# Optimization experiments

Measured on AMD Instinct MI355X. Metric: run time of the kernel, lower is better.

The kernel has to match this reference:

```python
import jax, jax.numpy as jnp
import numpy as np

B, S, D = 2, 4096, 1024

def setup_inputs() -> dict:
    key = jax.random.key(0)
    k1, k2 = jax.random.split(key)
    x = jax.random.normal(k1, (B, S, D), dtype=jnp.float32)
    W = jax.random.normal(k2, (D, 3 * D), dtype=jnp.float32) * (1.0 / np.sqrt(D))
    b = jnp.zeros((3 * D,), dtype=jnp.float32)
    return {"x": x, "W": W, "b": b}

def reference(x, W, b) -> jnp.ndarray:
    D_ = x.shape[-1]
    qkv = x @ W + b                       # [B, S, 3D]
    q, k, v = jnp.split(qkv, 3, axis=2)    # each [B, S, D]
    scale = 1.0 / jnp.sqrt(jnp.asarray(D_, dtype=x.dtype))
    scores = jnp.einsum('bqd,bkd->bqk', q, k) * scale  # [B, S, S]
    weights = jax.nn.softmax(scores, axis=-1)
    return jnp.einsum('bqk,bkd->bqd', weights, v)       # [B, S, D]
```

## Files before the change

### kernel.cpp

```cpp
#include <hip/hip_runtime.h>
#include <hip/hip_bf16.h>

typedef __attribute__((ext_vector_type(4))) float  f32x4;
typedef __attribute__((ext_vector_type(8))) __bf16 bf16x8;
typedef __attribute__((ext_vector_type(8))) unsigned short u16x8;

typedef const __attribute__((address_space(1))) void gas_void;
typedef __attribute__((address_space(3))) void las_void;

__device__ __forceinline__ unsigned short f2bf(float x) {
    unsigned u = __builtin_bit_cast(unsigned, x);
    u += 0x7fffu + ((u >> 16) & 1u);
    return (unsigned short)(u >> 16);
}
__device__ __forceinline__ float bf2f(unsigned short h) {
    unsigned u = ((unsigned)h) << 16;
    return __builtin_bit_cast(float, u);
}
__device__ __forceinline__ void gload_lds16(const void* g, void* l) {
    __builtin_amdgcn_global_load_lds((gas_void*)g, (las_void*)l, 16, 0, 0);
}

#define WAITVM(N) asm volatile("s_waitcnt vmcnt(" #N ")" ::: "memory")
#define BAR() do { __builtin_amdgcn_s_barrier(); __builtin_amdgcn_sched_barrier(0); } while (0)

__global__ void k_f32_to_bf16(const float* __restrict__ in,
                              unsigned short* __restrict__ out, int n4) {
    int i = blockIdx.x * blockDim.x + threadIdx.x;
    if (i < n4) {
        float4 v = ((const float4*)in)[i];
        ushort4 o;
        o.x = f2bf(v.x); o.y = f2bf(v.y); o.z = f2bf(v.z); o.w = f2bf(v.w);
        ((ushort4*)out)[i] = o;
    }
}

__global__ void k_transpose_w(const float* __restrict__ W,
                              unsigned short* __restrict__ Wt,
                              int K, int N) {
    __shared__ unsigned short tile[32][33];
    int n0 = blockIdx.x * 32, k0 = blockIdx.y * 32;
    int tx = threadIdx.x, ty = threadIdx.y;
#pragma unroll
    for (int i = 0; i < 4; i++) {
        int kk = ty + i * 8;
        tile[kk][tx] = f2bf(W[(size_t)(k0 + kk) * N + n0 + tx]);
    }
    __syncthreads();
#pragma unroll
    for (int i = 0; i < 4; i++) {
        int nn = ty + i * 8;
        Wt[(size_t)(n0 + nn) * K + k0 + tx] = tile[tx][nn];
    }
}

__global__ __launch_bounds__(256, 2) void k_g128qkv(
        const unsigned short* __restrict__ A, int lda,
        const unsigned short* __restrict__ Bt, int ldb,
        unsigned short* __restrict__ C,
        unsigned short* __restrict__ Vt,
        const float* __restrict__ bias, int K) {
    __shared__ __align__(16) unsigned short As[2][8192];
    __shared__ __align__(16) unsigned short Bs[2][8192];

    const int nwg  = gridDim.x * gridDim.y;
    const int flat = blockIdx.y * gridDim.x + blockIdx.x;
    const int swzb = (flat & 7) * (nwg >> 3) + (flat >> 3);
    const int m0   = (swzb / gridDim.x) * 128;
    const int n0   = (swzb % gridDim.x) * 128;

    const int tid  = threadIdx.x;
    const int lane = tid & 63;
    const int wid  = tid >> 6;
    const int wr   = wid >> 1;
    const int wc   = wid & 1;
    const int l15  = lane & 15;
    const int l4   = lane >> 4;

    f32x4 acc[4][4] = {};

    const int srow = tid >> 3;
    const int kel  = (((lane & 7) ^ (lane >> 3)) << 3);
    const int c0 = (l4 << 4) ^ ((l15 & 7) << 4);
    const int c1 = (64 + (l4 << 4)) ^ ((l15 & 7) << 4);

    auto stA = [&](int b, int g, int kt) {
        gload_lds16(A + (size_t)(m0 + g * 32 + srow) * lda + kt * 64 + kel,
                    (char*)As + b * 16384 + g * 4096 + (wid << 10));
    };
    auto stB = [&](int b, int g, int kt) {
        gload_lds16(Bt + (size_t)(n0 + g * 32 + srow) * ldb + kt * 64 + kel,
                    (char*)Bs + b * 16384 + g * 4096 + (wid << 10));
    };

#define MM(I, J, X, Y) \
    acc[I][J] = __builtin_amdgcn_mfma_f32_16x16x32_bf16((X), (Y), acc[I][J], 0, 0, 0)

    const int NT = K >> 6;
    stA(0, 0, 0); stA(0, 1, 0); stA(0, 2, 0); stA(0, 3, 0);
    stB(0, 0, 0); stB(0, 1, 0); stB(0, 2, 0); stB(0, 3, 0);

    for (int t = 0; t < NT; t++) {
        const int cur = t & 1, nxt = cur ^ 1;
        const char* Ab = (const char*)As + cur * 16384;
        const char* Bb = (const char*)Bs + cur * 16384;
        const bool hn = (t + 1 < NT);

        bf16x8 af[4], bq[4];

        if (hn) {
            stA(nxt, 0, t + 1); stA(nxt, 1, t + 1); stA(nxt, 2, t + 1); stA(nxt, 3, t + 1);
            WAITVM(4);
        } else {
            WAITVM(0);
        }
        BAR();
#pragma unroll
        for (int mf = 0; mf < 4; mf++)
            af[mf] = *(const bf16x8*)(Ab + (wr * 64 + mf * 16 + l15) * 128 + c0);
#pragma unroll
        for (int nf = 0; nf < 4; nf++)
            bq[nf] = *(const bf16x8*)(Bb + (wc * 64 + nf * 16 + l15) * 128 + c0);
        __builtin_amdgcn_s_setprio(1);
#pragma unroll
        for (int mf = 0; mf < 4; mf++)
#pragma unroll
        for (int nf = 0; nf < 4; nf++)
            MM(mf, nf, af[mf], bq[nf]);
        __builtin_amdgcn_s_setprio(0);

        if (hn) {
            stB(nxt, 0, t + 1); stB(nxt, 1, t + 1); stB(nxt, 2, t + 1); stB(nxt, 3, t + 1);
        }
#pragma unroll
        for (int mf = 0; mf < 4; mf++)
            af[mf] = *(const bf16x8*)(Ab + (wr * 64 + mf * 16 + l15) * 128 + c1);
#pragma unroll
        for (int nf = 0; nf < 4; nf++)
            bq[nf] = *(const bf16x8*)(Bb + (wc * 64 + nf * 16 + l15) * 128 + c1);
        __builtin_amdgcn_s_setprio(1);
#pragma unroll
        for (int mf = 0; mf < 4; mf++)
#pragma unroll
        for (int nf = 0; nf < 4; nf++)
            MM(mf, nf, af[mf], bq[nf]);
        __builtin_amdgcn_s_setprio(0);
        BAR();
    }
#undef MM

#pragma unroll
    for (int mf = 0; mf < 4; mf++) {
        const int row = m0 + wr * 64 + mf * 16 + l4 * 4;
#pragma unroll
        for (int nf = 0; nf < 4; nf++) {
            const int col = n0 + wc * 64 + nf * 16 + l15;
            const f32x4 av = acc[mf][nf];
            const float bv = bias[col];
            const int lc = col & 1023;
            if (col < 2048) {
#pragma unroll
                for (int r = 0; r < 4; r++)
                    C[(size_t)(col >> 10) * 8388608 +
                      (size_t)(row + r) * 1024 + lc] = f2bf(av[r] + bv);
            } else {
                const int b = row >> 12, s = row & 4095;
                ushort4 o;
                o.x = f2bf(av[0] + bv); o.y = f2bf(av[1] + bv);
                o.z = f2bf(av[2] + bv); o.w = f2bf(av[3] + bv);
                *(ushort4*)&Vt[(size_t)b * 4194304 + (size_t)lc * 4096 + s] = o;
            }
        }
    }
}

__global__ __launch_bounds__(512, 2) void k_scores(
        const unsigned short* __restrict__ A,
        const unsigned short* __restrict__ Bt,
        unsigned short* __restrict__ C,
        float* __restrict__ part,
        int K, float scale, long sA, long sB, long sC) {
    __shared__ __align__(16) unsigned short As[2][16384];
    __shared__ __align__(16) unsigned short Bs[2][16384];

    const int z = blockIdx.z;
    A  += (size_t)z * sA;
    Bt += (size_t)z * sB;

    const int nwg  = gridDim.x * gridDim.y;
    const int flat = blockIdx.y * gridDim.x + blockIdx.x;
    const int swzb = (flat & 7) * (nwg >> 3) + (flat >> 3);
    const int m0   = (swzb / gridDim.x) * 256;
    const int n0   = (swzb % gridDim.x) * 256;

    const int tid  = threadIdx.x;
    const int lane = tid & 63;
    const int wid  = tid >> 6;
    const int wm   = wid >> 2;
    const int wn   = wid & 3;
    const int l15  = lane & 15;
    const int l4   = lane >> 4;

    f32x4 acc[8][4] = {};

    const int srow = tid >> 3;
    const int kel  = (((lane & 7) ^ (lane >> 3)) << 3);
    const int c0 = ((l4 << 4)) ^ ((l15 & 7) << 4);
    const int c1 = (64 + (l4 << 4)) ^ ((l15 & 7) << 4);

    auto stageA = [&](int b, int h, int kt) {
#pragma unroll
        for (int c = 0; c < 2; c++) {
            const int r = h * 128 + c * 64 + srow;
            gload_lds16(A + (size_t)(m0 + r) * 1024 + kt * 64 + kel,
                        (char*)As + b * 32768 + h * 16384 + c * 8192 + (wid << 10));
        }
    };
    auto stageB = [&](int b, int h, int kt) {
#pragma unroll
        for (int c = 0; c < 2; c++) {
            const int r = h * 128 + c * 64 + srow;
            gload_lds16(Bt + (size_t)(n0 + r) * 1024 + kt * 64 + kel,
                        (char*)Bs + b * 32768 + h * 16384 + c * 8192 + (wid << 10));
        }
    };

#define MM(I, J, X, Y) \
    acc[I][J] = __builtin_amdgcn_mfma_f32_16x16x32_bf16((X), (Y), acc[I][J], 0, 0, 0)

    const int NT = K >> 6;
    stageA(0, 0, 0); stageB(0, 0, 0); stageA(0, 1, 0); stageB(0, 1, 0);

    for (int t = 0; t < NT; t++) {
        const int cur = t & 1, nxt = cur ^ 1;
        const char* Ab = (const char*)As + cur * 32768;
        const char* Bb = (const char*)Bs + cur * 32768;

        if (t + 1 < NT) {
            stageA(nxt, 0, t + 1); stageB(nxt, 0, t + 1);
            WAITVM(4);
        } else {
            WAITVM(0);
        }
        BAR();

        bf16x8 bfrg[2][2][2];
#pragma unroll
        for (int qn = 0; qn < 2; qn++)
#pragma unroll
        for (int nf = 0; nf < 2; nf++) {
            const int rb = (wn * 64 + qn * 32 + nf * 16 + l15) * 128;
            bfrg[qn][nf][0] = *(const bf16x8*)(Bb + rb + c0);
            bfrg[qn][nf][1] = *(const bf16x8*)(Bb + rb + c1);
        }
        {
            bf16x8 af[4][2];
#pragma unroll
            for (int mf = 0; mf < 4; mf++) {
                const int ra = (wm * 128 + 0 * 64 + mf * 16 + l15) * 128;
                af[mf][0] = *(const bf16x8*)(Ab + ra + c0);
                af[mf][1] = *(const bf16x8*)(Ab + ra + c1);
            }
            __builtin_amdgcn_s_setprio(1);
#pragma unroll
            for (int mf = 0; mf < 4; mf++)
#pragma unroll
            for (int qn = 0; qn < 2; qn++)
#pragma unroll
            for (int nf = 0; nf < 2; nf++) {
                MM(mf, qn * 2 + nf, af[mf][0], bfrg[qn][nf][0]);
                MM(mf, qn * 2 + nf, af[mf][1], bfrg[qn][nf][1]);
            }
            __builtin_amdgcn_s_setprio(0);
        }

        if (t + 1 < NT) { stageA(nxt, 1, t + 1); stageB(nxt, 1, t + 1); }
        {
            bf16x8 af[4][2];
#pragma unroll
            for (int mf = 0; mf < 4; mf++) {
                const int ra = (wm * 128 + 1 * 64 + mf * 16 + l15) * 128;
                af[mf][0] = *(const bf16x8*)(Ab + ra + c0);
                af[mf][1] = *(const bf16x8*)(Ab + ra + c1);
            }
            __builtin_amdgcn_s_setprio(1);
#pragma unroll
            for (int mf = 0; mf < 4; mf++)
#pragma unroll
            for (int qn = 0; qn < 2; qn++)
#pragma unroll
            for (int nf = 0; nf < 2; nf++) {
                MM(4 + mf, qn * 2 + nf, af[mf][0], bfrg[qn][nf][0]);
                MM(4 + mf, qn * 2 + nf, af[mf][1], bfrg[qn][nf][1]);
            }
            __builtin_amdgcn_s_setprio(0);
        }
        __builtin_amdgcn_s_barrier();
        __builtin_amdgcn_sched_barrier(0);
    }
#undef MM

    const int cb4 = ((n0 >> 8) << 2) + wn;
#pragma unroll
    for (int qm = 0; qm < 2; qm++)
#pragma unroll
    for (int mf = 0; mf < 4; mf++) {
        const int row = m0 + wm * 128 + qm * 64 + mf * 16 + l4 * 4;
        float rs[4] = {0.f, 0.f, 0.f, 0.f};
#pragma unroll
        for (int qn = 0; qn < 2; qn++)
#pragma unroll
        for (int nf = 0; nf < 2; nf++) {
            const int col = n0 + wn * 64 + qn * 32 + nf * 16 + l15;
            const f32x4 av = acc[qm * 4 + mf][qn * 2 + nf];
#pragma unroll
            for (int r = 0; r < 4; r++) {
                const float e = __expf(av[r] * scale);
                rs[r] += e;
                C[(size_t)z * sC + (size_t)(row + r) * 4096 + col] = f2bf(e);
            }
        }
#pragma unroll
        for (int r = 0; r < 4; r++) {
#pragma unroll
            for (int o = 1; o < 16; o <<= 1)
                rs[r] += __shfl_xor(rs[r], o);
        }
        if (l15 == 0) {
#pragma unroll
            for (int r = 0; r < 4; r++)
                part[((size_t)z * 4096 + row + r) * 64 + cb4] = rs[r];
        }
    }
}

__global__ __launch_bounds__(256) void k_rinv(const float* __restrict__ part,
                                              float* __restrict__ rinv, int nrows) {
    int row = blockIdx.x * blockDim.x + threadIdx.x;
    if (row < nrows) {
        const float* p = part + (size_t)row * 64;
        float s = 0.f;
#pragma unroll
        for (int i = 0; i < 16; i++) {
            f32x4 v = *(const f32x4*)(p + i * 4);
            s += v[0] + v[1] + v[2] + v[3];
        }
        rinv[row] = 1.0f / s;
    }
}

__global__ __launch_bounds__(512, 2) void k_pv256(
        const unsigned short* __restrict__ A,
        const unsigned short* __restrict__ Bt,
        float* __restrict__ C,
        const float* __restrict__ rinv,
        int K, long sA, long sB, long sC) {
    __shared__ __align__(16) unsigned short As[2][16384];
    __shared__ __align__(16) unsigned short Bs[2][8192];

    const int z = blockIdx.z;
    A  += (size_t)z * sA;
    Bt += (size_t)z * sB;

    const int nwg  = gridDim.x * gridDim.y;
    const int flat = blockIdx.y * gridDim.x + blockIdx.x;
    const int swzb = (flat & 7) * (nwg >> 3) + (flat >> 3);
    const int m0   = (swzb / gridDim.x) * 256;
    const int n0   = (swzb % gridDim.x) * 128;

    const int tid  = threadIdx.x;
    const int lane = tid & 63;
    const int wid  = tid >> 6;
    const int wm   = wid >> 2;
    const int wn   = wid & 3;
    const int l15  = lane & 15;
    const int l4   = lane >> 4;

    f32x4 acc[8][2] = {};

    const int srow = tid >> 3;
    const int kel  = (((lane & 7) ^ (lane >> 3)) << 3);
    const int c0 = ((l4 << 4)) ^ ((l15 & 7) << 4);
    const int c1 = (64 + (l4 << 4)) ^ ((l15 & 7) << 4);

    auto stageA1 = [&](int b, int a, int kt) {
        const int r = a * 64 + srow;
        gload_lds16(A + (size_t)(m0 + r) * 4096 + kt * 64 + kel,
                    (char*)As + b * 32768 + a * 8192 + (wid << 10));
    };
    auto stageB1 = [&](int b, int c, int kt) {
        const int r = c * 64 + srow;
        gload_lds16(Bt + (size_t)(n0 + r) * 4096 + kt * 64 + kel,
                    (char*)Bs + b * 16384 + c * 8192 + (wid << 10));
    };

#define MM(I, J, X, Y) \
    acc[I][J] = __builtin_amdgcn_mfma_f32_16x16x32_bf16((X), (Y), acc[I][J], 0, 0, 0)

    const int NT = K >> 6;
    stageA1(0, 0, 0); stageA1(0, 1, 0); stageA1(0, 2, 0); stageA1(0, 3, 0);
    stageB1(0, 0, 0); stageB1(0, 1, 0);

    for (int t = 0; t < NT; t++) {
        const int cur = t & 1, nxt = cur ^ 1;
        const char* Ab = (const char*)As + cur * 32768;
        const char* Bb = (const char*)Bs + cur * 16384;

        if (t + 1 < NT) {
            stageA1(nxt, 0, t + 1); stageA1(nxt, 1, t + 1); stageB1(nxt, 0, t + 1);
            WAITVM(3);
        } else {
            WAITVM(0);
        }
        BAR();

        bf16x8 bfrg[2][2];
#pragma unroll
        for (int nf = 0; nf < 2; nf++) {
            const int rb = (wn * 32 + nf * 16 + l15) * 128;
            bfrg[nf][0] = *(const bf16x8*)(Bb + rb + c0);
            bfrg[nf][1] = *(const bf16x8*)(Bb + rb + c1);
        }
        {
            bf16x8 af[4][2];
#pragma unroll
            for (int mf = 0; mf < 4; mf++) {
                const int ra = (wm * 128 + 0 * 64 + mf * 16 + l15) * 128;
                af[mf][0] = *(const bf16x8*)(Ab + ra + c0);
                af[mf][1] = *(const bf16x8*)(Ab + ra + c1);
            }
            __builtin_amdgcn_s_setprio(1);
#pragma unroll
            for (int mf = 0; mf < 4; mf++)
#pragma unroll
            for (int nf = 0; nf < 2; nf++) {
                MM(mf, nf, af[mf][0], bfrg[nf][0]);
                MM(mf, nf, af[mf][1], bfrg[nf][1]);
            }
            __builtin_amdgcn_s_setprio(0);
        }

        if (t + 1 < NT) {
            stageA1(nxt, 2, t + 1); stageA1(nxt, 3, t + 1); stageB1(nxt, 1, t + 1);
        }
        {
            bf16x8 af[4][2];
#pragma unroll
            for (int mf = 0; mf < 4; mf++) {
                const int ra = (wm * 128 + 1 * 64 + mf * 16 + l15) * 128;
                af[mf][0] = *(const bf16x8*)(Ab + ra + c0);
                af[mf][1] = *(const bf16x8*)(Ab + ra + c1);
            }
            __builtin_amdgcn_s_setprio(1);
#pragma unroll
            for (int mf = 0; mf < 4; mf++)
#pragma unroll
            for (int nf = 0; nf < 2; nf++) {
                MM(4 + mf, nf, af[mf][0], bfrg[nf][0]);
                MM(4 + mf, nf, af[mf][1], bfrg[nf][1]);
            }
            __builtin_amdgcn_s_setprio(0);
        }
        __builtin_amdgcn_s_barrier();
        __builtin_amdgcn_sched_barrier(0);
    }
#undef MM

#pragma unroll
    for (int qm = 0; qm < 2; qm++)
#pragma unroll
    for (int mf = 0; mf < 4; mf++) {
        const int row = m0 + wm * 128 + qm * 64 + mf * 16 + l4 * 4;
        const f32x4 riv = *(const f32x4*)&rinv[(size_t)z * 4096 + row];
#pragma unroll
        for (int nf = 0; nf < 2; nf++) {
            const int col = n0 + wn * 32 + nf * 16 + l15;
            const f32x4 av = acc[qm * 4 + mf][nf];
#pragma unroll
            for (int r = 0; r < 4; r++)
                C[(size_t)z * sC + (size_t)(row + r) * 1024 + col] = av[r] * riv[r];
        }
    }
}

extern "C" void kernel_launch(void* const* d_in, const int* in_sizes, int n_in,
                              void* d_out, int out_size, void* d_ws, size_t ws_size,
                              hipStream_t stream) {
    const float* x    = (const float*)d_in[0];
    const float* W    = (const float*)d_in[1];
    const float* bias = (const float*)d_in[2];
    float* out        = (float*)d_out;

    char* ws = (char*)d_ws;
    unsigned short* Qb   = (unsigned short*)(ws);
    unsigned short* Vt   = (unsigned short*)(ws + 33554432);
    unsigned short* xb   = (unsigned short*)(ws + 50331648);
    unsigned short* Wt   = (unsigned short*)(ws + 67108864);
    unsigned short* Pcat = (unsigned short*)(ws + 50331648);
    float*          part = (float*)(ws + 117440512);
    float*          rinv = (float*)(ws + 121634816);

    k_f32_to_bf16<<<8192, 256, 0, stream>>>(x, xb, (8192 * 1024) / 4);
    k_transpose_w<<<dim3(96, 32), dim3(32, 8), 0, stream>>>(W, Wt, 1024, 3072);
    k_g128qkv<<<dim3(24, 64), 256, 0, stream>>>(xb, 1024, Wt, 1024, Qb, Vt, bias, 1024);

    const float scale = 0.03125f;
    k_scores<<<dim3(16, 16, 2), 512, 0, stream>>>(
        Qb, Qb + 8388608, Pcat, part, 1024, scale, 4194304, 4194304, 16777216);
    k_rinv<<<32, 256, 0, stream>>>(part, rinv, 8192);
    k_pv256<<<dim3(8, 16, 2), 512, 0, stream>>>(
        Pcat, Vt, out, rinv, 4096, 16777216, 4194304, 4194304);
}
```

Baseline: 266.1 us.

## Restructure scores GEMM main loop into eight-phase interleaved load/compute schedule

Replaces the two-half double-buffered k-loop of the QK^T scores kernel with an 8-phase schedule over two k-tiles per iteration. Each phase computes one quadrant of the output tile while a slice of the next tiles is staged into LDS. The LDS staging layout is remapped so each half-buffer holds the rows a quadrant needs. This aims to spread global-to-LDS loads evenly across MFMA work and hide memory latency better. The cost is more barriers per k-step, and correctness depends on the new buffer and waitcnt bookkeeping.

Measured after the change: 272.1 us. 1.02x slower.

```diff
diff --git a/kernel.cpp b/kernel.cpp
--- a/kernel.cpp
+++ b/kernel.cpp
@@ -174,7 +174,7 @@
     }
 }
 
-__global__ __launch_bounds__(512, 2) void k_scores(
+__global__ __launch_bounds__(512, 2) void k_scores8(
         const unsigned short* __restrict__ A,
         const unsigned short* __restrict__ Bt,
         unsigned short* __restrict__ C,
@@ -203,102 +203,86 @@
 
     f32x4 acc[8][4] = {};
 
-    const int srow = tid >> 3;
-    const int kel  = (((lane & 7) ^ (lane >> 3)) << 3);
-    const int c0 = ((l4 << 4)) ^ ((l15 & 7) << 4);
+    const int kel = (((lane & 7) ^ (lane >> 3)) << 3);
+    const int c0 = (l4 << 4) ^ ((l15 & 7) << 4);
     const int c1 = (64 + (l4 << 4)) ^ ((l15 & 7) << 4);
 
-    auto stageA = [&](int b, int h, int kt) {
+    auto stA = [&](int b, int h, int kt) {
 #pragma unroll
         for (int c = 0; c < 2; c++) {
-            const int r = h * 128 + c * 64 + srow;
-            gload_lds16(A + (size_t)(m0 + r) * 1024 + kt * 64 + kel,
+            const int r = c * 64 + (tid >> 3);
+            const int grow = m0 + ((r >> 6) << 7) + h * 64 + (r & 63);
+            gload_lds16(A + (size_t)grow * 1024 + kt * 64 + kel,
                         (char*)As + b * 32768 + h * 16384 + c * 8192 + (wid << 10));
         }
     };
-    auto stageB = [&](int b, int h, int kt) {
+    auto stB = [&](int b, int h, int kt) {
 #pragma unroll
         for (int c = 0; c < 2; c++) {
-            const int r = h * 128 + c * 64 + srow;
-            gload_lds16(Bt + (size_t)(n0 + r) * 1024 + kt * 64 + kel,
+            const int r = c * 64 + (tid >> 3);
+            const int gcol = n0 + (((r >> 5) & 3) << 6) + h * 32 + (r & 31);
+            gload_lds16(Bt + (size_t)gcol * 1024 + kt * 64 + kel,
                         (char*)Bs + b * 32768 + h * 16384 + c * 8192 + (wid << 10));
         }
     };
 
-#define MM(I, J, X, Y) \
+#define MMp(I, J, X, Y) \
     acc[I][J] = __builtin_amdgcn_mfma_f32_16x16x32_bf16((X), (Y), acc[I][J], 0, 0, 0)
 
-    const int NT = K >> 6;
-    stageA(0, 0, 0); stageB(0, 0, 0); stageA(0, 1, 0); stageB(0, 1, 0);
-
-    for (int t = 0; t < NT; t++) {
-        const int cur = t & 1, nxt = cur ^ 1;
-        const char* Ab = (const char*)As + cur * 32768;
-        const char* Bb = (const char*)Bs + cur * 32768;
-
-        if (t + 1 < NT) {
-            stageA(nxt, 0, t + 1); stageB(nxt, 0, t + 1);
-            WAITVM(4);
-        } else {
-            WAITVM(0);
-        }
-        BAR();
-
-        bf16x8 bfrg[2][2][2];
-#pragma unroll
-        for (int qn = 0; qn < 2; qn++)
-#pragma unroll
-        for (int nf = 0; nf < 2; nf++) {
-            const int rb = (wn * 64 + qn * 32 + nf * 16 + l15) * 128;
-            bfrg[qn][nf][0] = *(const bf16x8*)(Bb + rb + c0);
-            bfrg[qn][nf][1] = *(const bf16x8*)(Bb + rb + c1);
-        }
-        {
-            bf16x8 af[4][2];
-#pragma unroll
-            for (int mf = 0; mf < 4; mf++) {
-                const int ra = (wm * 128 + 0 * 64 + mf * 16 + l15) * 128;
-                af[mf][0] = *(const bf16x8*)(Ab + ra + c0);
-                af[mf][1] = *(const bf16x8*)(Ab + ra + c1);
-            }
-            __builtin_amdgcn_s_setprio(1);
-#pragma unroll
-            for (int mf = 0; mf < 4; mf++)
-#pragma unroll
-            for (int qn = 0; qn < 2; qn++)
-#pragma unroll
-            for (int nf = 0; nf < 2; nf++) {
-                MM(mf, qn * 2 + nf, af[mf][0], bfrg[qn][nf][0]);
-                MM(mf, qn * 2 + nf, af[mf][1], bfrg[qn][nf][1]);
-            }
-            __builtin_amdgcn_s_setprio(0);
-        }
-
-        if (t + 1 < NT) { stageA(nxt, 1, t + 1); stageB(nxt, 1, t + 1); }
-        {
-            bf16x8 af[4][2];
-#pragma unroll
-            for (int mf = 0; mf < 4; mf++) {
-                const int ra = (wm * 128 + 1 * 64 + mf * 16 + l15) * 128;
-                af[mf][0] = *(const bf16x8*)(Ab + ra + c0);
-                af[mf][1] = *(const bf16x8*)(Ab + ra + c1);
-            }
-            __builtin_amdgcn_s_setprio(1);
-#pragma unroll
-            for (int mf = 0; mf < 4; mf++)
-#pragma unroll
-            for (int qn = 0; qn < 2; qn++)
-#pragma unroll
-            for (int nf = 0; nf < 2; nf++) {
-                MM(4 + mf, qn * 2 + nf, af[mf][0], bfrg[qn][nf][0]);
-                MM(4 + mf, qn * 2 + nf, af[mf][1], bfrg[qn][nf][1]);
-            }
-            __builtin_amdgcn_s_setprio(0);
-        }
-        __builtin_amdgcn_s_barrier();
-        __builtin_amdgcn_sched_barrier(0);
-    }
-#undef MM
+#define PHASE(BUF, QM, QN, STG, GATE)                                          \
+    do {                                                                       \
+        const char* Ab = (const char*)As + (BUF) * 32768 + (QM) * 16384;       \
+        const char* Bb = (const char*)Bs + (BUF) * 32768 + (QN) * 16384;       \
+        bf16x8 af[4][2], bq[2][2];                                             \
+        _Pragma("unroll")                                                      \
+        for (int mf = 0; mf < 4; mf++) {                                       \
+            const int ra = (wm * 64 + mf * 16 + l15) * 128;                    \
+            af[mf][0] = *(const bf16x8*)(Ab + ra + c0);                        \
+            af[mf][1] = *(const bf16x8*)(Ab + ra + c1);                        \
+        }                                                                      \
+        _Pragma("unroll")                                                      \
+        for (int nf = 0; nf < 2; nf++) {                                       \
+            const int rb = (wn * 32 + nf * 16 + l15) * 128;                    \
+            bq[nf][0] = *(const bf16x8*)(Bb + rb + c0);                        \
+            bq[nf][1] = *(const bf16x8*)(Bb + rb + c1);                        \
+        }                                                                      \
+        STG;                                                                   \
+        GATE;                                                                  \
+        __builtin_amdgcn_s_barrier();                                          \
+        asm volatile("s_waitcnt lgkmcnt(0)" ::: "memory");                     \
+        __builtin_amdgcn_sched_barrier(0);                                     \
+        __builtin_amdgcn_s_setprio(1);                                         \
+        _Pragma("unroll")                                                      \
+        for (int mf = 0; mf < 4; mf++)                                         \
+        _Pragma("unroll")                                                      \
+        for (int nf = 0; nf < 2; nf++) {                                       \
+            MMp((QM) * 4 + mf, (QN) * 2 + nf, af[mf][0], bq[nf][0]);           \
+            MMp((QM) * 4 + mf, (QN) * 2 + nf, af[mf][1], bq[nf][1]);           \
+        }                                                                      \
+        __builtin_amdgcn_s_setprio(0);                                         \
+        __builtin_amdgcn_s_barrier();                                          \
+    } while (0)
+
+    const int NITER = K >> 7;
+    stA(0, 0, 0); stB(0, 0, 0); stA(0, 1, 0); stB(0, 1, 0);
+    stA(1, 0, 1); stB(1, 0, 1);
+    WAITVM(4);
+    __builtin_amdgcn_s_barrier();
+
+    for (int j = 0; j < NITER; j++) {
+        const bool hn = (j + 1 < NITER);
+        const int t1 = 2 * j + 1, t2 = 2 * j + 2, t3 = 2 * j + 3;
+        PHASE(0, 0, 0, stA(1, 1, t1), (void)0);
+        PHASE(0, 0, 1, stB(1, 1, t1), (void)0);
+        PHASE(0, 1, 0, if (hn) stA(0, 0, t2), (void)0);
+        PHASE(0, 1, 1, if (hn) stB(0, 0, t2), if (hn) WAITVM(4); else WAITVM(0));
+        PHASE(1, 0, 0, if (hn) stA(0, 1, t2), (void)0);
+        PHASE(1, 0, 1, if (hn) stB(0, 1, t2), (void)0);
+        PHASE(1, 1, 0, if (hn) stA(1, 0, t3), (void)0);
+        PHASE(1, 1, 1, if (hn) stB(1, 0, t3), if (hn) WAITVM(4));
+    }
+#undef PHASE
+#undef MMp
 
     const int cb4 = ((n0 >> 8) << 2) + wn;
 #pragma unroll
@@ -505,7 +489,7 @@
     k_g128qkv<<<dim3(24, 64), 256, 0, stream>>>(xb, 1024, Wt, 1024, Qb, Vt, bias, 1024);
 
     const float scale = 0.03125f;
-    k_scores<<<dim3(16, 16, 2), 512, 0, stream>>>(
+    k_scores8<<<dim3(16, 16, 2), 512, 0, stream>>>(
         Qb, Qb + 8388608, Pcat, part, 1024, scale, 4194304, 4194304, 16777216);
     k_rinv<<<32, 256, 0, stream>>>(part, rinv, 8192);
     k_pv256<<<dim3(8, 16, 2), 512, 0, stream>>>(
```
